# Optimization experiments

Measured on AMD Instinct MI355X. Metric: run time of the kernel, lower is better.

The kernel has to match this reference:

```python
import jax, jax.numpy as jnp
import numpy as np

B, H, W, DIM = 8, 56, 56, 512
WS, SS, HEADS = 7, 3, 16
HD = DIM // HEADS
NW_TOK = WS * WS  # 49 tokens per window


def _make_mask():
    # static additive attention mask for shifted windows (numpy, concrete)
    img = np.zeros((H, W), dtype=np.float32)
    slices = [slice(0, -WS), slice(-WS, -SS), slice(-SS, None)]
    cnt = 0
    for hs in slices:
        for ws_ in slices:
            img[hs, ws_] = cnt
            cnt += 1
    m = img.reshape(H // WS, WS, W // WS, WS).transpose(0, 2, 1, 3).reshape(-1, NW_TOK)
    diff = m[:, None, :] - m[:, :, None]
    return np.where(diff != 0, -np.inf, 0.0).astype(np.float32)  # (nW, 49, 49)

_MASK = jnp.asarray(_make_mask())


def _ln(x, w, b, eps=1e-5):
    mu = jnp.mean(x, axis=-1, keepdims=True)
    var = jnp.mean(jnp.square(x - mu), axis=-1, keepdims=True)
    return (x - mu) * jax.lax.rsqrt(var + eps) * w + b


def setup_inputs() -> dict:
    key = jax.random.key(0)
    ks = jax.random.split(key, 5)
    s = lambda fan: 1.0 / np.sqrt(fan)
    return {
        "x": jax.random.normal(ks[0], (B, H * W, DIM), jnp.float32),
        "ln1_w": jnp.ones((DIM,), jnp.float32),
        "ln1_b": jnp.zeros((DIM,), jnp.float32),
        "qkv_w": jax.random.normal(ks[1], (DIM, 3 * DIM), jnp.float32) * s(DIM),
        "qkv_b": jnp.zeros((3 * DIM,), jnp.float32),
        "proj_w": jax.random.normal(ks[2], (DIM, DIM), jnp.float32) * s(DIM),
        "proj_b": jnp.zeros((DIM,), jnp.float32),
        "ln2_w": jnp.ones((DIM,), jnp.float32),
        "ln2_b": jnp.zeros((DIM,), jnp.float32),
        "fc1_w": jax.random.normal(ks[3], (DIM, 2 * DIM), jnp.float32) * s(DIM),
        "fc1_b": jnp.zeros((2 * DIM,), jnp.float32),
        "fc2_w": jax.random.normal(ks[4], (2 * DIM, DIM), jnp.float32) * s(2 * DIM),
        "fc2_b": jnp.zeros((DIM,), jnp.float32),
    }


def reference(x, ln1_w, ln1_b, qkv_w, qkv_b, proj_w, proj_b, ln2_w, ln2_b, fc1_w, fc1_b, fc2_w, fc2_b):
    Bn = x.shape[0]
    xr = x.reshape(Bn, H, W, DIM)
    h = xr
    y = _ln(xr, ln1_w, ln1_b)
    y = jnp.roll(y, shift=(-SS, -SS), axis=(1, 2))
    # window partition: (Bn*nW, 49, DIM)
    win = y.reshape(Bn, H // WS, WS, W // WS, WS, DIM).transpose(0, 1, 3, 2, 4, 5)
    win = win.reshape(-1, NW_TOK, DIM)
    nWtot = win.shape[0]
    # window attention
    qkv = (win @ qkv_w + qkv_b).reshape(nWtot, NW_TOK, 3, HEADS, HD)
    q, k, v = (qkv[:, :, i].transpose(0, 2, 1, 3) for i in range(3))  # (nWtot, heads, 49, hd)
    attn = jnp.einsum('whqd,whkd->whqk', q * (HD ** -0.5), k)
    nW = _MASK.shape[0]
    attn = attn.reshape(Bn, nW, HEADS, NW_TOK, NW_TOK) + _MASK[None, :, None]
    attn = jax.nn.softmax(attn, axis=-1).reshape(nWtot, HEADS, NW_TOK, NW_TOK)
    out = jnp.einsum('whqk,whkd->whqd', attn, v)
    out = out.transpose(0, 2, 1, 3).reshape(nWtot, NW_TOK, DIM)
    out = out @ proj_w + proj_b
    # window reverse
    out = out.reshape(Bn, H // WS, W // WS, WS, WS, DIM).transpose(0, 1, 3, 2, 4, 5)
    out = out.reshape(Bn, H, W, DIM)
    out = jnp.roll(out, shift=(SS, SS), axis=(1, 2))
    x2 = (h + out).reshape(Bn, H * W, DIM)
    # MLP block
    z = _ln(x2, ln2_w, ln2_b)
    z = jax.nn.gelu(z @ fc1_w + fc1_b) @ fc2_w + fc2_b
    return x2 + z
```

## Files before the change

### kernel.cpp

```cpp
#include <hip/hip_runtime.h>

typedef unsigned short u16;
typedef unsigned short u16x8 __attribute__((ext_vector_type(8)));
typedef __bf16         bf16x8 __attribute__((ext_vector_type(8)));
typedef float          f32x4  __attribute__((ext_vector_type(4)));

#define DIM 512
#define LTOK 25088

__device__ __forceinline__ float bf2f(u16 u) {
  union { unsigned int i; float f; } c; c.i = ((unsigned int)u) << 16; return c.f;
}
__device__ __forceinline__ u16 f2bf(float f) {
  union { float f; unsigned int i; } c; c.f = f;
  unsigned int i = c.i;
  return (u16)((i + 0x7FFFu + ((i >> 16) & 1u)) >> 16);
}
__device__ __forceinline__ float gelu_tanh(float x) {
  float x3 = x * x * x;
  return 0.5f * x * (1.0f + tanhf(0.7978845608028654f * (x + 0.044715f * x3)));
}
__device__ __forceinline__ void gload16(const u16* g, u16* l) {
  __builtin_amdgcn_global_load_lds(
      (__attribute__((address_space(1))) void*)(u16*)g,
      (__attribute__((address_space(3))) void*)l,
      16, 0, 0);
}
__device__ __forceinline__ int rowToToken(int row) {
  int win = row / 49, t = row - win * 49;
  int b = win >> 6, wi = win & 63;
  int hr = (wi >> 3) * 7 + t / 7;
  int wr = (wi & 7) * 7 + t % 7;
  int hs = hr + 3; if (hs >= 56) hs -= 56;
  int ws2 = wr + 3; if (ws2 >= 56) ws2 -= 56;
  return b * 3136 + hs * 56 + ws2;
}

__global__ __launch_bounds__(256) void ln1_kernel(const float* __restrict__ x,
    const float* __restrict__ w, const float* __restrict__ b, u16* __restrict__ out) {
  int r = blockIdx.x * 4 + (threadIdx.x >> 6);
  int lane = threadIdx.x & 63;
  int tok = rowToToken(r);
  const float* src = x + (size_t)tok * DIM + lane * 8;
  float v[8]; float s = 0.f, ss = 0.f;
  f32x4 v0 = *(const f32x4*)(src);
  f32x4 v1 = *(const f32x4*)(src + 4);
  #pragma unroll
  for (int j = 0; j < 4; ++j) { v[j] = v0[j]; v[j + 4] = v1[j]; }
  #pragma unroll
  for (int j = 0; j < 8; ++j) { s += v[j]; ss += v[j] * v[j]; }
  #pragma unroll
  for (int off = 32; off > 0; off >>= 1) { s += __shfl_xor(s, off); ss += __shfl_xor(ss, off); }
  float mean = s * (1.0f / 512.0f);
  float var  = ss * (1.0f / 512.0f) - mean * mean;
  float rstd = rsqrtf(var + 1e-5f);
  f32x4 w0 = *(const f32x4*)(w + lane * 8), w1 = *(const f32x4*)(w + lane * 8 + 4);
  f32x4 b0 = *(const f32x4*)(b + lane * 8), b1 = *(const f32x4*)(b + lane * 8 + 4);
  u16x8 o;
  #pragma unroll
  for (int j = 0; j < 4; ++j) {
    o[j]     = f2bf((v[j]     - mean) * rstd * w0[j] + b0[j]);
    o[j + 4] = f2bf((v[j + 4] - mean) * rstd * w1[j] + b1[j]);
  }
  *(u16x8*)(out + (size_t)r * DIM + lane * 8) = o;
}

__global__ __launch_bounds__(256) void ln2_kernel(const float* __restrict__ x2,
    const float* __restrict__ w, const float* __restrict__ b, u16* __restrict__ out) {
  int r = blockIdx.x * 4 + (threadIdx.x >> 6);
  int lane = threadIdx.x & 63;
  const float* src = x2 + (size_t)r * DIM + lane * 8;
  float v[8]; float s = 0.f, ss = 0.f;
  f32x4 v0 = *(const f32x4*)(src);
  f32x4 v1 = *(const f32x4*)(src + 4);
  #pragma unroll
  for (int j = 0; j < 4; ++j) { v[j] = v0[j]; v[j + 4] = v1[j]; }
  #pragma unroll
  for (int j = 0; j < 8; ++j) { s += v[j]; ss += v[j] * v[j]; }
  #pragma unroll
  for (int off = 32; off > 0; off >>= 1) { s += __shfl_xor(s, off); ss += __shfl_xor(ss, off); }
  float mean = s * (1.0f / 512.0f);
  float var  = ss * (1.0f / 512.0f) - mean * mean;
  float rstd = rsqrtf(var + 1e-5f);
  f32x4 w0 = *(const f32x4*)(w + lane * 8), w1 = *(const f32x4*)(w + lane * 8 + 4);
  f32x4 b0 = *(const f32x4*)(b + lane * 8), b1 = *(const f32x4*)(b + lane * 8 + 4);
  u16x8 o;
  #pragma unroll
  for (int j = 0; j < 4; ++j) {
    o[j]     = f2bf((v[j]     - mean) * rstd * w0[j] + b0[j]);
    o[j + 4] = f2bf((v[j + 4] - mean) * rstd * w1[j] + b1[j]);
  }
  *(u16x8*)(out + (size_t)r * DIM + lane * 8) = o;
}

__global__ __launch_bounds__(256) void transpose_kernel(const float* __restrict__ in,
    u16* __restrict__ out, int K, int N) {
  __shared__ u16 tile[32][33];
  int tx = threadIdx.x & 31, ty = threadIdx.x >> 5;
  int n0 = blockIdx.x * 32, k0 = blockIdx.y * 32;
  #pragma unroll
  for (int r = 0; r < 4; ++r) {
    int kr = ty + r * 8;
    tile[kr][tx] = f2bf(in[(size_t)(k0 + kr) * N + n0 + tx]);
  }
  __syncthreads();
  #pragma unroll
  for (int r = 0; r < 4; ++r) {
    int nr = ty + r * 8;
    out[(size_t)(n0 + nr) * K + k0 + tx] = tile[tx][nr];
  }
}

template<int MODE, int N, int KD>
__global__ __launch_bounds__(256) void gemm_kernel(
    const u16* __restrict__ A, const u16* __restrict__ Bt,
    const float* __restrict__ bias, void* outp,
    const float* resF) {
  __shared__ __align__(16) u16 lA[128 * 64];
  __shared__ __align__(16) u16 lB[128 * 64];
  int tid = threadIdx.x;
  int lane = tid & 63, wid = tid >> 6;
  int wm = wid >> 1, wn = wid & 1;
  int m0 = blockIdx.x * 128, n0 = blockIdx.y * 128;
  int l15 = lane & 15, l4 = lane >> 4;
  f32x4 acc[4][4];
  #pragma unroll
  for (int i = 0; i < 4; ++i)
    #pragma unroll
    for (int j = 0; j < 4; ++j) acc[i][j] = (f32x4){0.f, 0.f, 0.f, 0.f};

  for (int k0 = 0; k0 < KD; k0 += 64) {
    #pragma unroll
    for (int is = 0; is < 4; ++is) {
      int e = is * 2048 + tid * 8;
      int mm = e >> 6, kk = e & 63;
      gload16(A  + (size_t)(m0 + mm) * KD + k0 + kk, &lA[is * 2048 + wid * 512]);
      gload16(Bt + (size_t)(n0 + mm) * KD + k0 + kk, &lB[is * 2048 + wid * 512]);
    }
    __syncthreads();
    #pragma unroll
    for (int ks = 0; ks < 2; ++ks) {
      bf16x8 af[4], bfv[4];
      #pragma unroll
      for (int i = 0; i < 4; ++i)
        af[i] = *(const bf16x8*)&lA[(wm * 64 + i * 16 + l15) * 64 + ks * 32 + l4 * 8];
      #pragma unroll
      for (int j = 0; j < 4; ++j)
        bfv[j] = *(const bf16x8*)&lB[(wn * 64 + j * 16 + l15) * 64 + ks * 32 + l4 * 8];
      #pragma unroll
      for (int i = 0; i < 4; ++i)
        #pragma unroll
        for (int j = 0; j < 4; ++j)
          acc[i][j] = __builtin_amdgcn_mfma_f32_16x16x32_bf16(af[i], bfv[j], acc[i][j], 0, 0, 0);
    }
    __syncthreads();
  }

  #pragma unroll
  for (int i = 0; i < 4; ++i) {
    #pragma unroll
    for (int j = 0; j < 4; ++j) {
      int col = n0 + wn * 64 + j * 16 + l15;
      float bcol = bias[col];
      #pragma unroll
      for (int r = 0; r < 4; ++r) {
        int row = m0 + wm * 64 + i * 16 + l4 * 4 + r;
        float v = acc[i][j][r] + bcol;
        if constexpr (MODE == 0) {
          ((u16*)outp)[(size_t)row * N + col] = f2bf(v);
        } else if constexpr (MODE == 1) {
          int tok = rowToToken(row);
          size_t idx = (size_t)tok * DIM + col;
          ((float*)outp)[idx] = v + resF[idx];
        } else if constexpr (MODE == 2) {
          ((u16*)outp)[(size_t)row * N + col] = f2bf(gelu_tanh(v));
        } else {
          size_t idx = (size_t)row * N + col;
          ((float*)outp)[idx] = v + resF[idx];
        }
      }
    }
  }
}

__global__ __launch_bounds__(256) void attn_kernel(const u16* __restrict__ qkv,
                                                   u16* __restrict__ out) {
  int win = blockIdx.x;
  int wi = win & 63;
  int tid = threadIdx.x, lane = tid & 63, wid = tid >> 6;
  int l15 = lane & 15, l4 = lane >> 4;
  __shared__ int codes[49];
  __shared__ __align__(16) u16 plds[4][64 * 72];
  if (tid < 49) {
    int hr = (wi >> 3) * 7 + tid / 7;
    int wr = (wi & 7) * 7 + tid % 7;
    int rh = (hr < 49) ? 0 : (hr < 53 ? 1 : 2);
    int rw = (wr < 49) ? 0 : (wr < 53 ? 1 : 2);
    codes[tid] = rh * 3 + rw;
  }
  __syncthreads();
  int ck[4], cq[4][4];
  #pragma unroll
  for (int j = 0; j < 4; ++j) {
    int c = 16 * j + l15;
    ck[j] = (c < 49) ? codes[c] : -1;
  }
  #pragma unroll
  for (int i = 0; i < 4; ++i)
    #pragma unroll
    for (int r = 0; r < 4; ++r) {
      int row = 16 * i + 4 * l4 + r;
      cq[i][r] = codes[row < 49 ? row : 48];
    }
  size_t wbase = (size_t)win * 49 * 1536;
  u16* pw = plds[wid];
  const float scale = 0.17677669529663687f;

  for (int hh = 0; hh < 4; ++hh) {
    int head = wid * 4 + hh;
    size_t hoff = wbase + (size_t)head * 32;

    bf16x8 vf[2][2];
    #pragma unroll
    for (int ks = 0; ks < 2; ++ks)
      #pragma unroll
      for (int jn = 0; jn < 2; ++jn) {
        u16x8 tmp;
        #pragma unroll
        for (int j = 0; j < 8; ++j) {
          int tok = ks * 32 + l4 * 8 + j; tok = tok < 49 ? tok : 48;
          tmp[j] = qkv[hoff + (size_t)tok * 1536 + 1024 + jn * 16 + l15];
        }
        vf[ks][jn] = __builtin_bit_cast(bf16x8, tmp);
      }

    bf16x8 qf[4], kf[4];
    #pragma unroll
    for (int i = 0; i < 4; ++i) {
      int tr = 16 * i + l15; tr = tr < 49 ? tr : 48;
      qf[i] = *(const bf16x8*)(qkv + hoff + (size_t)tr * 1536 + l4 * 8);
      kf[i] = *(const bf16x8*)(qkv + hoff + (size_t)tr * 1536 + 512 + l4 * 8);
    }

    f32x4 acc[4][4];
    #pragma unroll
    for (int i = 0; i < 4; ++i)
      #pragma unroll
      for (int j = 0; j < 4; ++j) acc[i][j] = (f32x4){0.f, 0.f, 0.f, 0.f};
    #pragma unroll
    for (int i = 0; i < 4; ++i)
      #pragma unroll
      for (int j = 0; j < 4; ++j)
        acc[i][j] = __builtin_amdgcn_mfma_f32_16x16x32_bf16(qf[i], kf[j], acc[i][j], 0, 0, 0);

    #pragma unroll
    for (int i = 0; i < 4; ++i) {
      #pragma unroll
      for (int r = 0; r < 4; ++r) {
        float s0[4];
        float m = -1e30f;
        #pragma unroll
        for (int j = 0; j < 4; ++j) {
          float s_ = acc[i][j][r] * scale;
          s_ = (ck[j] == cq[i][r]) ? s_ : -1e30f;
          s0[j] = s_;
          m = fmaxf(m, s_);
        }
        m = fmaxf(m, __shfl_xor(m, 1));
        m = fmaxf(m, __shfl_xor(m, 2));
        m = fmaxf(m, __shfl_xor(m, 4));
        m = fmaxf(m, __shfl_xor(m, 8));
        float sum = 0.f;
        #pragma unroll
        for (int j = 0; j < 4; ++j) { s0[j] = __expf(s0[j] - m); sum += s0[j]; }
        sum += __shfl_xor(sum, 1);
        sum += __shfl_xor(sum, 2);
        sum += __shfl_xor(sum, 4);
        sum += __shfl_xor(sum, 8);
        float inv = 1.0f / sum;
        int row = 16 * i + 4 * l4 + r;
        #pragma unroll
        for (int j = 0; j < 4; ++j)
          pw[row * 72 + 16 * j + l15] = f2bf(s0[j] * inv);
      }
    }

    f32x4 oacc[4][2];
    #pragma unroll
    for (int i = 0; i < 4; ++i)
      #pragma unroll
      for (int jn = 0; jn < 2; ++jn) oacc[i][jn] = (f32x4){0.f, 0.f, 0.f, 0.f};
    #pragma unroll
    for (int ks = 0; ks < 2; ++ks) {
      bf16x8 pf[4];
      #pragma unroll
      for (int i = 0; i < 4; ++i)
        pf[i] = *(const bf16x8*)&pw[(16 * i + l15) * 72 + ks * 32 + l4 * 8];
      #pragma unroll
      for (int i = 0; i < 4; ++i)
        #pragma unroll
        for (int jn = 0; jn < 2; ++jn)
          oacc[i][jn] = __builtin_amdgcn_mfma_f32_16x16x32_bf16(pf[i], vf[ks][jn], oacc[i][jn], 0, 0, 0);
    }

    #pragma unroll
    for (int i = 0; i < 4; ++i) {
      int row = 16 * i + 4 * l4;
      #pragma unroll
      for (int jn = 0; jn < 2; ++jn)
        #pragma unroll
        for (int r = 0; r < 4; ++r)
          if (row + r < 49)
            out[((size_t)win * 49 + row + r) * 512 + head * 32 + jn * 16 + l15] =
                f2bf(oacc[i][jn][r]);
    }
  }
}

extern "C" void kernel_launch(void* const* d_in, const int* in_sizes, int n_in,
                              void* d_out, int out_size, void* d_ws, size_t ws_size,
                              hipStream_t stream) {
  const float* x     = (const float*)d_in[0];
  const float* ln1w  = (const float*)d_in[1];
  const float* ln1b  = (const float*)d_in[2];
  const float* qkvw  = (const float*)d_in[3];
  const float* qkvb  = (const float*)d_in[4];
  const float* projw = (const float*)d_in[5];
  const float* projb = (const float*)d_in[6];
  const float* ln2w  = (const float*)d_in[7];
  const float* ln2b  = (const float*)d_in[8];
  const float* fc1w  = (const float*)d_in[9];
  const float* fc1b  = (const float*)d_in[10];
  const float* fc2w  = (const float*)d_in[11];
  const float* fc2b  = (const float*)d_in[12];
  float* outF = (float*)d_out;

  u16* wsu     = (u16*)d_ws;
  u16* qkv_wt  = wsu;
  u16* proj_wt = qkv_wt  + 512 * 1536;
  u16* fc1_wt  = proj_wt + 512 * 512;
  u16* fc2_wt  = fc1_wt  + 512 * 1024;
  u16* xw      = fc2_wt  + 1024 * 512;
  u16* qkvB    = xw + (size_t)LTOK * 512;
  u16* attnO   = xw;
  u16* z_in    = xw;
  u16* z1      = qkvB;
  float* x2    = outF;

  transpose_kernel<<<dim3(1536 / 32, 512 / 32), 256, 0, stream>>>(qkvw, qkv_wt, 512, 1536);
  transpose_kernel<<<dim3(512 / 32, 512 / 32),  256, 0, stream>>>(projw, proj_wt, 512, 512);
  transpose_kernel<<<dim3(1024 / 32, 512 / 32), 256, 0, stream>>>(fc1w, fc1_wt, 512, 1024);
  transpose_kernel<<<dim3(512 / 32, 1024 / 32), 256, 0, stream>>>(fc2w, fc2_wt, 1024, 512);

  ln1_kernel<<<LTOK / 4, 256, 0, stream>>>(x, ln1w, ln1b, xw);

  gemm_kernel<0, 1536, 512><<<dim3(196, 12), 256, 0, stream>>>(xw, qkv_wt, qkvb, qkvB, nullptr);

  attn_kernel<<<512, 256, 0, stream>>>(qkvB, attnO);

  gemm_kernel<1, 512, 512><<<dim3(196, 4), 256, 0, stream>>>(attnO, proj_wt, projb, x2, x);

  ln2_kernel<<<LTOK / 4, 256, 0, stream>>>(x2, ln2w, ln2b, z_in);

  gemm_kernel<2, 1024, 512><<<dim3(196, 8), 256, 0, stream>>>(z_in, fc1_wt, fc1b, z1, nullptr);

  gemm_kernel<3, 512, 1024><<<dim3(196, 4), 256, 0, stream>>>(z1, fc2_wt, fc2b, outF, x2);
}
```

Before: 469.7 us.

## Double-buffer GEMM LDS tiles with XOR swizzle, MFMA priority, and cheaper GELU

```diff
diff --git a/kernel.cpp b/kernel.cpp
--- a/kernel.cpp
+++ b/kernel.cpp
@@ -17,8 +17,9 @@
   return (u16)((i + 0x7FFFu + ((i >> 16) & 1u)) >> 16);
 }
 __device__ __forceinline__ float gelu_tanh(float x) {
-  float x3 = x * x * x;
-  return 0.5f * x * (1.0f + tanhf(0.7978845608028654f * (x + 0.044715f * x3)));
+  float x2 = x * x;
+  float y2 = x * (1.5957691216057308f + 0.0713548162726f * x2);
+  return x / (1.0f + __expf(-y2));
 }
 __device__ __forceinline__ void gload16(const u16* g, u16* l) {
   __builtin_amdgcn_global_load_lds(
@@ -116,8 +117,8 @@
     const u16* __restrict__ A, const u16* __restrict__ Bt,
     const float* __restrict__ bias, void* outp,
     const float* resF) {
-  __shared__ __align__(16) u16 lA[128 * 64];
-  __shared__ __align__(16) u16 lB[128 * 64];
+  __shared__ __align__(16) u16 lA[2][8192];
+  __shared__ __align__(16) u16 lB[2][8192];
   int tid = threadIdx.x;
   int lane = tid & 63, wid = tid >> 6;
   int wm = wid >> 1, wn = wid & 1;
@@ -129,32 +130,47 @@
     #pragma unroll
     for (int j = 0; j < 4; ++j) acc[i][j] = (f32x4){0.f, 0.f, 0.f, 0.f};
 
-  for (int k0 = 0; k0 < KD; k0 += 64) {
+  auto stage = [&](int buf, int k0) {
     #pragma unroll
     for (int is = 0; is < 4; ++is) {
       int e = is * 2048 + tid * 8;
-      int mm = e >> 6, kk = e & 63;
-      gload16(A  + (size_t)(m0 + mm) * KD + k0 + kk, &lA[is * 2048 + wid * 512]);
-      gload16(Bt + (size_t)(n0 + mm) * KD + k0 + kk, &lB[is * 2048 + wid * 512]);
-    }
-    __syncthreads();
+      int mm = e >> 6;
+      int kk = (e & 63) ^ ((mm & 7) << 3);
+      gload16(A  + (size_t)(m0 + mm) * KD + k0 + kk, &lA[buf][is * 2048 + wid * 512]);
+      gload16(Bt + (size_t)(n0 + mm) * KD + k0 + kk, &lB[buf][is * 2048 + wid * 512]);
+    }
+  };
+  auto compute = [&](int buf) {
     #pragma unroll
     for (int ks = 0; ks < 2; ++ks) {
       bf16x8 af[4], bfv[4];
+      int ksw = (ks * 32 + l4 * 8) ^ ((l15 & 7) << 3);
       #pragma unroll
       for (int i = 0; i < 4; ++i)
-        af[i] = *(const bf16x8*)&lA[(wm * 64 + i * 16 + l15) * 64 + ks * 32 + l4 * 8];
+        af[i] = *(const bf16x8*)&lA[buf][(wm * 64 + i * 16 + l15) * 64 + ksw];
       #pragma unroll
       for (int j = 0; j < 4; ++j)
-        bfv[j] = *(const bf16x8*)&lB[(wn * 64 + j * 16 + l15) * 64 + ks * 32 + l4 * 8];
+        bfv[j] = *(const bf16x8*)&lB[buf][(wn * 64 + j * 16 + l15) * 64 + ksw];
+      __builtin_amdgcn_s_setprio(1);
       #pragma unroll
       for (int i = 0; i < 4; ++i)
         #pragma unroll
         for (int j = 0; j < 4; ++j)
           acc[i][j] = __builtin_amdgcn_mfma_f32_16x16x32_bf16(af[i], bfv[j], acc[i][j], 0, 0, 0);
-    }
+      __builtin_amdgcn_s_setprio(0);
+    }
+  };
+
+  stage(0, 0);
+  __syncthreads();
+  int cur = 0;
+  for (int t = 0; t < KD / 64 - 1; ++t) {
+    stage(cur ^ 1, (t + 1) * 64);
+    compute(cur);
     __syncthreads();
-  }
+    cur ^= 1;
+  }
+  compute(cur);
 
   #pragma unroll
   for (int i = 0; i < 4; ++i) {
```

Result: faster. 420.5 us (-10.5%).
